# Optimization experiments

Hardware: AMD Instinct MI355X
Metric: run time of the kernel (lower is better)

## Reference

```python
import jax, jax.numpy as jnp
import numpy as np

N = 50000
H = 300


def l2_normalize(x, eps=1e-12):
    n = jnp.sqrt(jnp.sum(x * x, axis=1, keepdims=True))
    return x / jnp.maximum(n, eps)


def gat_layer(x, ei_j, ei_i, a_i, a_j, n_nodes):
    # per-node scalar scores, gathered per edge
    s_i = x @ a_i  # [N]
    s_j = x @ a_j  # [N]
    e = jax.nn.leaky_relu(s_i[ei_i] + s_j[ei_j], 0.01)  # [E]
    # scatter softmax over incoming edges of node i
    m = jax.ops.segment_max(e, ei_i, num_segments=n_nodes)
    ex = jnp.exp(e - m[ei_i])
    denom = jax.ops.segment_sum(ex, ei_i, num_segments=n_nodes)
    alpha = ex / (denom[ei_i] + 1e-16)
    out = jax.ops.segment_sum(alpha[:, None] * x[ei_j], ei_i, num_segments=n_nodes)
    return jax.nn.relu(out)


def gcn_layer(x, ei_j, ei_i, W, n_nodes):
    deg = jax.ops.segment_sum(jnp.ones_like(ei_i, dtype=x.dtype), ei_i, num_segments=n_nodes)
    dinv = jnp.where(deg > 0, deg ** -0.5, 0.0)
    norm = dinv[ei_j] * dinv[ei_i]  # [E]
    h = x @ W.T
    out = jax.ops.segment_sum(norm[:, None] * h[ei_j], ei_i, num_segments=n_nodes)
    return jax.nn.relu(out)


def highway(x1, x2, W, b):
    gate = jax.nn.sigmoid(x1 @ W.T + b)
    return gate * x2 + (1.0 - gate) * x1


def setup_inputs() -> dict:
    key = jax.random.key(0)
    ks = jax.random.split(key, 16)
    s = 1.0 / np.sqrt(H)
    inp = {
        "x_e": jax.random.normal(ks[0], (N, H), dtype=jnp.float32),
        "edge_index": jax.random.randint(ks[1], (2, 400000), 0, N, dtype=jnp.int32),
        "rel": jax.random.randint(ks[2], (400000,), 0, 1000, dtype=jnp.int32),
        "edge_index_all": jax.random.randint(ks[3], (2, 800000), 0, N, dtype=jnp.int32),
        "rel_all": jax.random.randint(ks[4], (800000,), 0, 1000, dtype=jnp.int32),
        "gcn1_W": jax.random.uniform(ks[5], (H, H), jnp.float32, -s, s),
        "hw1_W": jax.random.uniform(ks[6], (H, H), jnp.float32, -s, s),
        "hw1_b": jax.random.uniform(ks[7], (H,), jnp.float32, -s, s),
        "gat1_ai": jax.random.uniform(ks[8], (H,), jnp.float32, -s, s),
        "gat1_aj": jax.random.uniform(ks[9], (H,), jnp.float32, -s, s),
        "ghw1_W": jax.random.uniform(ks[10], (H, H), jnp.float32, -s, s),
        "ghw1_b": jax.random.uniform(ks[11], (H,), jnp.float32, -s, s),
        "gat2_ai": jax.random.uniform(ks[12], (H,), jnp.float32, -s, s),
        "gat2_aj": jax.random.uniform(ks[13], (H,), jnp.float32, -s, s),
        "ghw2_W": jax.random.uniform(ks[14], (H, H), jnp.float32, -s, s),
        "ghw2_b": jax.random.uniform(ks[15], (H,), jnp.float32, -s, s),
    }
    k2 = jax.random.split(jax.random.key(1), 2)
    inp["gat_ai"] = jax.random.uniform(k2[0], (H,), jnp.float32, -s, s)
    inp["gat_aj"] = jax.random.uniform(k2[1], (H,), jnp.float32, -s, s)
    return inp


def reference(x_e, edge_index, rel, edge_index_all, rel_all,
              gcn1_W, hw1_W, hw1_b, gat1_ai, gat1_aj, ghw1_W, ghw1_b,
              gat2_ai, gat2_aj, ghw2_W, ghw2_b, gat_ai, gat_aj):
    # dropout(p=0.05) treated as identity (eval mode)
    ei_j, ei_i = edge_index_all[0], edge_index_all[1]
    n = x_e.shape[0]

    x0 = l2_normalize(x_e)
    x2 = highway(x0, gcn_layer(x0, ei_j, ei_i, gcn1_W, n), hw1_W, hw1_b)
    x3 = highway(x2, gat_layer(x2, ei_j, ei_i, gat1_ai, gat1_aj, n), ghw1_W, ghw1_b)
    xe = highway(x2, gat_layer(x3, ei_j, ei_i, gat2_ai, gat2_aj, n), ghw2_W, ghw2_b)
    ye = gat_layer(xe, ei_j, ei_i, gat_ai, gat_aj, n)
    return jnp.concatenate([xe, ye], axis=1)
```

## Files before the change

### kernel.cpp

```cpp
#include <hip/hip_runtime.h>
#include <hip/hip_bf16.h>
#include <math.h>

#define H 300
#define WAVE 64
#define STRB 320
#define SCB 1024

typedef short bf16x8 __attribute__((ext_vector_type(8)));
typedef unsigned short u16;
typedef u16 u16x8 __attribute__((ext_vector_type(8)));
typedef u16 u16x4 __attribute__((ext_vector_type(4)));
typedef float f32x4 __attribute__((ext_vector_type(4)));

__device__ inline unsigned short f2b(float f) {
    union { float f; unsigned int u; } x; x.f = f;
    unsigned int r = x.u + 0x7FFF + ((x.u >> 16) & 1);
    return (unsigned short)(r >> 16);
}
__device__ inline float b2f(u16 h) {
    union { float f; unsigned int u; } x; x.u = ((unsigned int)h) << 16;
    return x.f;
}

__global__ void k_l2norm(const float* __restrict__ x, u16* __restrict__ outb, int n) {
    int wave = blockIdx.x * (blockDim.x / WAVE) + (threadIdx.x >> 6);
    int lane = threadIdx.x & 63;
    if (wave >= n) return;
    const float* row = x + (long)wave * H;
    float s = 0.f;
    for (int j = lane; j < H; j += WAVE) { float v = row[j]; s += v * v; }
    for (int o = 32; o > 0; o >>= 1) s += __shfl_xor(s, o);
    float sc = 1.0f / fmaxf(sqrtf(s), 1e-12f);
    u16* brow = outb + (long)wave * STRB;
    for (int j = lane; j < H; j += WAVE) brow[j] = f2b(row[j] * sc);
    for (int j = H + lane; j < STRB; j += WAVE) brow[j] = 0;
}

__global__ void k_zero_int(int* p, int n) {
    int i = blockIdx.x * blockDim.x + threadIdx.x;
    int stride = gridDim.x * blockDim.x;
    for (; i < n; i += stride) p[i] = 0;
}

__global__ void k_count_deg(const int* __restrict__ ei_i, int* __restrict__ deg, int E) {
    int i = blockIdx.x * blockDim.x + threadIdx.x;
    int stride = gridDim.x * blockDim.x;
    for (; i < E; i += stride) atomicAdd(&deg[ei_i[i]], 1);
}

__global__ void k_scan_local(const int* __restrict__ deg, int* __restrict__ offs,
                             int* __restrict__ btot, float* __restrict__ dinv, int n) {
    __shared__ int sh[SCB];
    int base = blockIdx.x * SCB;
    int tid = threadIdx.x;
    int v = (base + tid < n) ? deg[base + tid] : 0;
    if (base + tid < n) dinv[base + tid] = (v > 0) ? 1.0f / sqrtf((float)v) : 0.0f;
    sh[tid] = v;
    __syncthreads();
    for (int off = 1; off < SCB; off <<= 1) {
        int add = (tid >= off) ? sh[tid - off] : 0;
        __syncthreads();
        sh[tid] += add;
        __syncthreads();
    }
    if (base + tid < n) offs[base + tid] = sh[tid] - v;
    if (tid == SCB - 1) btot[blockIdx.x] = sh[tid];
}

__global__ void k_scan_tots(const int* __restrict__ btot, int* __restrict__ bpre,
                            int nb, int* __restrict__ total_out) {
    int l = threadIdx.x;
    int v = (l < nb) ? btot[l] : 0;
    int own = v;
    for (int o = 1; o < 64; o <<= 1) {
        int u = __shfl_up(v, o);
        if (l >= o) v += u;
    }
    if (l < nb) bpre[l] = v - own;
    if (l == 63) total_out[0] = v;
}

__global__ void k_scan_apply(int* __restrict__ offs, const int* __restrict__ bpre,
                             int* __restrict__ cursor, int n) {
    int i = blockIdx.x * blockDim.x + threadIdx.x;
    int stride = gridDim.x * blockDim.x;
    for (; i < n; i += stride) {
        int o = offs[i] + bpre[i / SCB];
        offs[i] = o;
        cursor[i] = o;
    }
}

__global__ void k_fill_csr(const int* __restrict__ ei_j, const int* __restrict__ ei_i,
                           int* __restrict__ cursor, int* __restrict__ csr_src, int E) {
    int i = blockIdx.x * blockDim.x + threadIdx.x;
    int stride = gridDim.x * blockDim.x;
    for (; i < E; i += stride) {
        int dst = ei_i[i];
        int pos = atomicAdd(&cursor[dst], 1);
        csr_src[pos] = ei_j[i];
    }
}

__global__ void k_conv_w4(const float* __restrict__ W0f, const float* __restrict__ W1f,
                          const float* __restrict__ W2f, const float* __restrict__ W3f,
                          u16* __restrict__ Wb0, u16* __restrict__ Wb1,
                          u16* __restrict__ Wb2, u16* __restrict__ Wb3) {
    int which = blockIdx.x & 3;
    const float* W = (which == 0) ? W0f : (which == 1) ? W1f : (which == 2) ? W2f : W3f;
    u16* Wb = (which == 0) ? Wb0 : (which == 1) ? Wb1 : (which == 2) ? Wb2 : Wb3;
    int idx = (blockIdx.x >> 2) * blockDim.x + threadIdx.x;
    int stride = (gridDim.x >> 2) * blockDim.x;
    for (; idx < STRB * STRB; idx += stride) {
        int r = idx / STRB, c = idx - r * STRB;
        Wb[idx] = (r < H && c < H) ? f2b(W[r * H + c]) : 0;
    }
}

#define BM 128
#define BN 64
#define BK 32
#define LDP 40
#define STP 70
#define NXCD 8

__global__ __launch_bounds__(256) void k_gemm_fused(
        const u16* __restrict__ Xb,
        const u16* __restrict__ Wb,
        u16* __restrict__ outb,
        const float* __restrict__ hwbias,
        const u16* __restrict__ xnewb, const float* __restrict__ xnewf,
        const u16* __restrict__ xold,
        float* __restrict__ outf, long ostride,
        u16* __restrict__ mirror,
        int n_rows) {
    __shared__ __align__(16) char smem[BM * STP * 2];
    short* As = (short*)smem;
    short* Bs = (short*)(smem + BM * LDP * 2);
    u16*   St = (u16*)smem;
    const int tid = threadIdx.x;

    const int nwg = gridDim.x;
    const int q = nwg / NXCD, r = nwg % NXCD;
    const int xcd = blockIdx.x % NXCD, idx = blockIdx.x / NXCD;
    const int wgid = (xcd < r ? xcd * (q + 1) : r * (q + 1) + (xcd - r) * q) + idx;
    const int bm = (wgid / 5) * BM;
    const int bn = (wgid % 5) * BN;

    const int lane = tid & 63;
    const int wid = tid >> 6;
    const int wr = wid >> 1;
    const int wc = wid & 1;
    const int lrow = lane & 15;
    const int kgrp = lane >> 4;

    f32x4 acc[4][2];
    #pragma unroll
    for (int m = 0; m < 4; m++)
        #pragma unroll
        for (int n = 0; n < 2; n++) acc[m][n] = (f32x4){0.f, 0.f, 0.f, 0.f};

    for (int k0 = 0; k0 < STRB; k0 += BK) {
        #pragma unroll
        for (int i = 0; i < 2; ++i) {
            int qq = tid + i * 256;
            int rr = qq >> 2, c = (qq & 3) << 3;
            int gr = bm + rr;
            u16x8 v = {0, 0, 0, 0, 0, 0, 0, 0};
            if (gr < n_rows) v = *(const u16x8*)&Xb[(long)gr * STRB + k0 + c];
            *(u16x8*)&As[rr * LDP + c] = v;
        }
        {
            int rr = tid >> 2, c = (tid & 3) << 3;
            u16x8 v = *(const u16x8*)&Wb[(long)(bn + rr) * STRB + k0 + c];
            *(u16x8*)&Bs[rr * LDP + c] = v;
        }
        __syncthreads();

        bf16x8 af[4], bfr[2];
        #pragma unroll
        for (int m = 0; m < 4; m++) {
            int row = wr * 64 + m * 16 + lrow;
            af[m] = *(const bf16x8*)&As[row * LDP + kgrp * 8];
        }
        #pragma unroll
        for (int n = 0; n < 2; n++) {
            int col = wc * 32 + n * 16 + lrow;
            bfr[n] = *(const bf16x8*)&Bs[col * LDP + kgrp * 8];
        }
        #pragma unroll
        for (int m = 0; m < 4; m++)
            #pragma unroll
            for (int n = 0; n < 2; n++)
                acc[m][n] = __builtin_amdgcn_mfma_f32_16x16x32_bf16(af[m], bfr[n], acc[m][n], 0, 0, 0);
        __syncthreads();
    }

    #pragma unroll
    for (int m = 0; m < 4; m++)
        #pragma unroll
        for (int n = 0; n < 2; n++) {
            int lc = wc * 32 + n * 16 + lrow;
            #pragma unroll
            for (int rr = 0; rr < 4; rr++) {
                int row = wr * 64 + m * 16 + kgrp * 4 + rr;
                St[row * STP + lc] = f2b(acc[m][n][rr]);
            }
        }
    __syncthreads();

    #pragma unroll
    for (int p = 0; p < 4; p++) {
        int row = p * 32 + (tid >> 3);
        int gr = bm + row;
        if (gr >= n_rows) continue;
        int lc0 = (tid & 7) * 8;
        int gc0 = bn + lc0;
        u16x8 pv = *(const u16x8*)&St[row * STP + lc0];
        if (outb) {
            u16x8 o;
            #pragma unroll
            for (int j = 0; j < 8; j++) o[j] = (gc0 + j < H) ? pv[j] : (u16)0;
            *(u16x8*)&outb[(long)gr * STRB + gc0] = o;
        } else {
            u16x8 xov = *(const u16x8*)&xold[(long)gr * STRB + gc0];
            float xn[8];
            if (xnewb) {
                u16x8 xnv = *(const u16x8*)&xnewb[(long)gr * STRB + gc0];
                #pragma unroll
                for (int j = 0; j < 8; j++) xn[j] = b2f(xnv[j]);
            } else {
                f32x4 a = *(const f32x4*)&xnewf[(long)gr * H + gc0];
                f32x4 b = *(const f32x4*)&xnewf[(long)gr * H + gc0 + 4];
                xn[0] = a[0]; xn[1] = a[1]; xn[2] = a[2]; xn[3] = a[3];
                xn[4] = b[0]; xn[5] = b[1]; xn[6] = b[2]; xn[7] = b[3];
            }
            float val[8];
            #pragma unroll
            for (int j = 0; j < 8; j++) {
                int gcj = gc0 + j;
                if (gcj < H) {
                    float pre = b2f(pv[j]) + hwbias[gcj];
                    float g = 1.0f / (1.0f + __expf(-pre));
                    val[j] = g * xn[j] + (1.0f - g) * b2f(xov[j]);
                } else val[j] = 0.f;
            }
            if (outf) {
                if (gc0 < H)
                    *(f32x4*)&outf[(long)gr * ostride + gc0] = (f32x4){val[0], val[1], val[2], val[3]};
                if (gc0 + 4 < H)
                    *(f32x4*)&outf[(long)gr * ostride + gc0 + 4] = (f32x4){val[4], val[5], val[6], val[7]};
            }
            if (mirror) {
                u16x8 mv;
                #pragma unroll
                for (int j = 0; j < 8; j++) mv[j] = f2b(val[j]);
                *(u16x8*)&mirror[(long)gr * STRB + gc0] = mv;
            }
        }
    }
}

__global__ __launch_bounds__(256) void k_gcn_gather_w(const u16* __restrict__ xb,
                                                      const float* __restrict__ dinv,
                                                      const int* __restrict__ offs,
                                                      const int* __restrict__ csr,
                                                      u16* __restrict__ outb, int n) {
    int node = blockIdx.x * 4 + (threadIdx.x >> 6);
    int lane = threadIdx.x & 63;
    if (node >= n) return;
    int start = offs[node], end = offs[node + 1];
    float acc[8];
    #pragma unroll
    for (int j = 0; j < 8; j++) acc[j] = 0.f;
    float di = dinv[node];
    for (int tb = start; tb < end; tb += 64) {
        int p = tb + lane;
        int src = 0; float w = 0.f;
        if (p < end) {
            src = csr[p];
            w = di * dinv[src];
        }
        int cnt = min(64, end - tb);
        for (int qq = 0; qq < cnt; qq++) {
            float wq = __shfl(w, qq);
            int sq = __shfl(src, qq);
            if (lane < 40) {
                u16x8 v = *(const u16x8*)&xb[(long)sq * STRB + lane * 8];
                #pragma unroll
                for (int j = 0; j < 8; j++) acc[j] += wq * b2f(v[j]);
            }
        }
    }
    if (lane < 40) {
        u16x8 o;
        #pragma unroll
        for (int j = 0; j < 8; j++) o[j] = f2b(fmaxf(acc[j], 0.f));
        *(u16x8*)&outb[(long)node * STRB + lane * 8] = o;
    }
}

__global__ void k_dual_dot_b(const u16* __restrict__ xb,
                             const float* __restrict__ ai, const float* __restrict__ aj,
                             float* __restrict__ s_i, float* __restrict__ s_j, int n) {
    int wave = blockIdx.x * (blockDim.x / WAVE) + (threadIdx.x >> 6);
    int lane = threadIdx.x & 63;
    if (wave >= n) return;
    const u16* row = xb + (long)wave * STRB;
    float d0 = 0.f, d1 = 0.f;
    {
        u16x4 v = *(const u16x4*)&row[lane * 4];
        float4 a4 = *(const float4*)&ai[lane * 4];
        float4 j4 = *(const float4*)&aj[lane * 4];
        float x0 = b2f(v[0]), x1 = b2f(v[1]), x2 = b2f(v[2]), x3 = b2f(v[3]);
        d0 = x0 * a4.x + x1 * a4.y + x2 * a4.z + x3 * a4.w;
        d1 = x0 * j4.x + x1 * j4.y + x2 * j4.z + x3 * j4.w;
    }
    if (lane < 11) {
        u16x4 v = *(const u16x4*)&row[256 + lane * 4];
        float4 a4 = *(const float4*)&ai[256 + lane * 4];
        float4 j4 = *(const float4*)&aj[256 + lane * 4];
        float x0 = b2f(v[0]), x1 = b2f(v[1]), x2 = b2f(v[2]), x3 = b2f(v[3]);
        d0 += x0 * a4.x + x1 * a4.y + x2 * a4.z + x3 * a4.w;
        d1 += x0 * j4.x + x1 * j4.y + x2 * j4.z + x3 * j4.w;
    }
    for (int o = 32; o > 0; o >>= 1) { d0 += __shfl_down(d0, o); d1 += __shfl_down(d1, o); }
    if (lane == 0) { s_i[wave] = d0; s_j[wave] = d1; }
}

__global__ __launch_bounds__(256) void k_gat_gather_w(const u16* __restrict__ xb,
                                                      const float* __restrict__ s_i_arr,
                                                      const float* __restrict__ s_j_arr,
                                                      const int* __restrict__ offs,
                                                      const int* __restrict__ csr,
                                                      u16* __restrict__ outb16,
                                                      float* __restrict__ outf, long out_stride,
                                                      int out_off, int n) {
    int node = blockIdx.x * 4 + (threadIdx.x >> 6);
    int lane = threadIdx.x & 63;
    if (node >= n) return;
    int start = offs[node], end = offs[node + 1];
    int deg = end - start;
    float acc[8];
    #pragma unroll
    for (int j = 0; j < 8; j++) acc[j] = 0.f;

    if (deg > 0) {
        float si = s_i_arr[node];
        float m_t = -1e30f, s_t = 0.f;
        for (int p = start + lane; p < end; p += 64) {
            float sc = si + s_j_arr[csr[p]];
            sc = (sc >= 0.f) ? sc : 0.01f * sc;
            if (sc > m_t) { s_t = s_t * __expf(m_t - sc) + 1.0f; m_t = sc; }
            else s_t += __expf(sc - m_t);
        }
        for (int o = 32; o > 0; o >>= 1) {
            float m2 = __shfl_xor(m_t, o), s2 = __shfl_xor(s_t, o);
            float mm = fmaxf(m_t, m2);
            s_t = s_t * __expf(m_t - mm) + s2 * __expf(m2 - mm);
            m_t = mm;
        }
        float m = m_t;
        float inv = 1.0f / (s_t + 1e-16f);
        for (int tb = start; tb < end; tb += 64) {
            int p = tb + lane;
            int src = 0; float w = 0.f;
            if (p < end) {
                src = csr[p];
                float sc = si + s_j_arr[src];
                sc = (sc >= 0.f) ? sc : 0.01f * sc;
                w = __expf(sc - m) * inv;
            }
            int cnt = min(64, end - tb);
            for (int qq = 0; qq < cnt; qq++) {
                float wq = __shfl(w, qq);
                int sq = __shfl(src, qq);
                if (lane < 40) {
                    u16x8 v = *(const u16x8*)&xb[(long)sq * STRB + lane * 8];
                    #pragma unroll
                    for (int j = 0; j < 8; j++) acc[j] += wq * b2f(v[j]);
                }
            }
        }
    }
    if (outb16) {
        if (lane < 40) {
            u16x8 o;
            #pragma unroll
            for (int j = 0; j < 8; j++) o[j] = f2b(fmaxf(acc[j], 0.f));
            *(u16x8*)&outb16[(long)node * STRB + lane * 8] = o;
        }
    } else {
        if (lane < 38) {
            #pragma unroll
            for (int j = 0; j < 8; j++) {
                int c = lane * 8 + j;
                if (c < H) outf[(long)node * out_stride + out_off + c] = fmaxf(acc[j], 0.f);
            }
        }
    }
}

extern "C" void kernel_launch(void* const* d_in, const int* in_sizes, int n_in,
                              void* d_out, int out_size, void* d_ws, size_t ws_size,
                              hipStream_t stream) {
    const float* x_e     = (const float*)d_in[0];
    const int*   ei_all  = (const int*)d_in[3];
    const float* gcn1_W  = (const float*)d_in[5];
    const float* hw1_W   = (const float*)d_in[6];
    const float* hw1_b   = (const float*)d_in[7];
    const float* gat1_ai = (const float*)d_in[8];
    const float* gat1_aj = (const float*)d_in[9];
    const float* ghw1_W  = (const float*)d_in[10];
    const float* ghw1_b  = (const float*)d_in[11];
    const float* gat2_ai = (const float*)d_in[12];
    const float* gat2_aj = (const float*)d_in[13];
    const float* ghw2_W  = (const float*)d_in[14];
    const float* ghw2_b  = (const float*)d_in[15];
    const float* gat_ai  = (const float*)d_in[16];
    const float* gat_aj  = (const float*)d_in[17];

    const int N = in_sizes[0] / H;
    const int E = in_sizes[3] / 2;
    const int* ei_j = ei_all;
    const int* ei_i = ei_all + E;

    float* out = (float*)d_out;

    size_t NSB = (size_t)N * STRB;
    u16*   W0   = (u16*)d_ws;
    u16*   W1   = W0 + NSB;
    u16*   W2   = W1 + NSB;
    u16*   W3   = W2 + NSB;
    float* G2F  = (float*)d_ws;
    float* sbi  = (float*)(W3 + NSB);
    float* sbj  = sbi + N;
    float* dinv = sbj + N;
    int*   deg  = (int*)(dinv + N);
    int*   offs = deg + N;
    int*   cursor = offs + (N + 1);
    int*   csr  = cursor + N;
    int*   btot = csr + E;
    int*   bpre = btot + 64;
    u16*   wb0  = (u16*)(bpre + 64);
    u16*   wb1  = wb0 + STRB * STRB;
    u16*   wb2  = wb1 + STRB * STRB;
    u16*   wb3  = wb2 + STRB * STRB;

    dim3 blk256(256);
    int rowsPerBlock = 256 / WAVE;
    dim3 gridRows((N + rowsPerBlock - 1) / rowsPerBlock);
    dim3 gridNodeW((N + 3) / 4);
    dim3 gridE(2048);
    dim3 gridW(400);
    dim3 gridGemm(((N + BM - 1) / BM) * 5);
    int nScanB = (N + SCB - 1) / SCB;

    hipLaunchKernelGGL(k_l2norm, gridRows, blk256, 0, stream, x_e, W0, N);

    hipLaunchKernelGGL(k_zero_int, dim3(256), blk256, 0, stream, deg, N);
    hipLaunchKernelGGL(k_count_deg, gridE, blk256, 0, stream, ei_i, deg, E);
    hipLaunchKernelGGL(k_scan_local, dim3(nScanB), dim3(SCB), 0, stream, deg, offs, btot, dinv, N);
    hipLaunchKernelGGL(k_scan_tots, dim3(1), dim3(64), 0, stream, btot, bpre, nScanB, offs + N);
    hipLaunchKernelGGL(k_scan_apply, dim3(256), blk256, 0, stream, offs, bpre, cursor, N);
    hipLaunchKernelGGL(k_fill_csr, gridE, blk256, 0, stream, ei_j, ei_i, cursor, csr, E);
    hipLaunchKernelGGL(k_conv_w4, gridW, blk256, 0, stream,
                       gcn1_W, hw1_W, ghw1_W, ghw2_W, wb0, wb1, wb2, wb3);

    hipLaunchKernelGGL(k_gemm_fused, gridGemm, blk256, 0, stream,
                       W0, wb0, W1,
                       (const float*)nullptr, (const u16*)nullptr, (const float*)nullptr,
                       (const u16*)nullptr, (float*)nullptr, (long)0, (u16*)nullptr, N);

    hipLaunchKernelGGL(k_gcn_gather_w, gridNodeW, blk256, 0, stream, W1, dinv, offs, csr, W2, N);

    hipLaunchKernelGGL(k_gemm_fused, gridGemm, blk256, 0, stream,
                       W0, wb1, (u16*)nullptr,
                       hw1_b, W2, (const float*)nullptr, W0,
                       (float*)nullptr, (long)0, W3, N);

    hipLaunchKernelGGL(k_dual_dot_b, gridRows, blk256, 0, stream, W3, gat1_ai, gat1_aj, sbi, sbj, N);

    hipLaunchKernelGGL(k_gat_gather_w, gridNodeW, blk256, 0, stream, W3, sbi, sbj, offs, csr,
                       W1, (float*)nullptr, (long)0, 0, N);

    hipLaunchKernelGGL(k_gemm_fused, gridGemm, blk256, 0, stream,
                       W3, wb2, (u16*)nullptr,
                       ghw1_b, W1, (const float*)nullptr, W3,
                       (float*)nullptr, (long)0, W2, N);

    hipLaunchKernelGGL(k_dual_dot_b, gridRows, blk256, 0, stream, W2, gat2_ai, gat2_aj, sbi, sbj, N);

    hipLaunchKernelGGL(k_gat_gather_w, gridNodeW, blk256, 0, stream, W2, sbi, sbj, offs, csr,
                       (u16*)nullptr, G2F, (long)H, 0, N);

    hipLaunchKernelGGL(k_gemm_fused, gridGemm, blk256, 0, stream,
                       W3, wb3, (u16*)nullptr,
                       ghw2_b, (const u16*)nullptr, G2F, W3,
                       out, (long)(2 * H), W2, N);

    hipLaunchKernelGGL(k_dual_dot_b, gridRows, blk256, 0, stream, W2, gat_ai, gat_aj, sbi, sbj, N);

    hipLaunchKernelGGL(k_gat_gather_w, gridNodeW, blk256, 0, stream, W2, sbi, sbj, offs, csr,
                       (u16*)nullptr, out, (long)(2 * H), H, N);
}
```

Measured before the change: 693.0 us.

## Fuse GAT score dot products into GEMM epilogue and unroll gather loops

Computes the per-node attention scores s_i/s_j inside the highway GEMM epilogue via partial dot products, shuffle reductions and atomicAdd into zeroed buffers. This removes the separate dual-dot kernels that reread the bf16 feature matrix. The GCN and GAT neighbour gather loops are also unrolled by four so that several row loads are in flight at once. The cost is extra memsets, atomic traffic and higher register pressure in the gather kernels.

```diff
diff --git a/kernel.cpp b/kernel.cpp
--- a/kernel.cpp
+++ b/kernel.cpp
@@ -10,7 +10,6 @@
 typedef short bf16x8 __attribute__((ext_vector_type(8)));
 typedef unsigned short u16;
 typedef u16 u16x8 __attribute__((ext_vector_type(8)));
-typedef u16 u16x4 __attribute__((ext_vector_type(4)));
 typedef float f32x4 __attribute__((ext_vector_type(4)));
 
 __device__ inline unsigned short f2b(float f) {
@@ -134,6 +133,8 @@
         const u16* __restrict__ xold,
         float* __restrict__ outf, long ostride,
         u16* __restrict__ mirror,
+        const float* __restrict__ dai, const float* __restrict__ daj,
+        float* __restrict__ sbi, float* __restrict__ sbj,
         int n_rows) {
     __shared__ __align__(16) char smem[BM * STP * 2];
     short* As = (short*)smem;
@@ -258,6 +259,26 @@
                 for (int j = 0; j < 8; j++) mv[j] = f2b(val[j]);
                 *(u16x8*)&mirror[(long)gr * STRB + gc0] = mv;
             }
+            if (dai) {
+                float p0 = 0.f, p1 = 0.f;
+                #pragma unroll
+                for (int j = 0; j < 8; j++) {
+                    int gcj = gc0 + j;
+                    if (gcj < H) {
+                        p0 += val[j] * dai[gcj];
+                        p1 += val[j] * daj[gcj];
+                    }
+                }
+                #pragma unroll
+                for (int o = 4; o > 0; o >>= 1) {
+                    p0 += __shfl_down(p0, o);
+                    p1 += __shfl_down(p1, o);
+                }
+                if ((tid & 7) == 0) {
+                    atomicAdd(&sbi[gr], p0);
+                    atomicAdd(&sbj[gr], p1);
+                }
+            }
         }
     }
 }
@@ -275,6 +296,7 @@
     #pragma unroll
     for (int j = 0; j < 8; j++) acc[j] = 0.f;
     float di = dinv[node];
+    const u16* rowp = xb + lane * 8;
     for (int tb = start; tb < end; tb += 64) {
         int p = tb + lane;
         int src = 0; float w = 0.f;
@@ -283,11 +305,32 @@
             w = di * dinv[src];
         }
         int cnt = min(64, end - tb);
-        for (int qq = 0; qq < cnt; qq++) {
+        int qq = 0;
+        for (; qq + 4 <= cnt; qq += 4) {
+            float w0 = __shfl(w, qq), w1 = __shfl(w, qq + 1);
+            float w2 = __shfl(w, qq + 2), w3 = __shfl(w, qq + 3);
+            int s0 = __shfl(src, qq), s1 = __shfl(src, qq + 1);
+            int s2 = __shfl(src, qq + 2), s3 = __shfl(src, qq + 3);
+            if (lane < 40) {
+                u16x8 v0 = *(const u16x8*)&rowp[(long)s0 * STRB];
+                u16x8 v1 = *(const u16x8*)&rowp[(long)s1 * STRB];
+                u16x8 v2 = *(const u16x8*)&rowp[(long)s2 * STRB];
+                u16x8 v3 = *(const u16x8*)&rowp[(long)s3 * STRB];
+                #pragma unroll
+                for (int j = 0; j < 8; j++) acc[j] += w0 * b2f(v0[j]);
+                #pragma unroll
+                for (int j = 0; j < 8; j++) acc[j] += w1 * b2f(v1[j]);
+                #pragma unroll
+                for (int j = 0; j < 8; j++) acc[j] += w2 * b2f(v2[j]);
+                #pragma unroll
+                for (int j = 0; j < 8; j++) acc[j] += w3 * b2f(v3[j]);
+            }
+        }
+        for (; qq < cnt; qq++) {
             float wq = __shfl(w, qq);
             int sq = __shfl(src, qq);
             if (lane < 40) {
-                u16x8 v = *(const u16x8*)&xb[(long)sq * STRB + lane * 8];
+                u16x8 v = *(const u16x8*)&rowp[(long)sq * STRB];
                 #pragma unroll
                 for (int j = 0; j < 8; j++) acc[j] += wq * b2f(v[j]);
             }
@@ -299,34 +342,6 @@
         for (int j = 0; j < 8; j++) o[j] = f2b(fmaxf(acc[j], 0.f));
         *(u16x8*)&outb[(long)node * STRB + lane * 8] = o;
     }
-}
-
-__global__ void k_dual_dot_b(const u16* __restrict__ xb,
-                             const float* __restrict__ ai, const float* __restrict__ aj,
-                             float* __restrict__ s_i, float* __restrict__ s_j, int n) {
-    int wave = blockIdx.x * (blockDim.x / WAVE) + (threadIdx.x >> 6);
-    int lane = threadIdx.x & 63;
-    if (wave >= n) return;
-    const u16* row = xb + (long)wave * STRB;
-    float d0 = 0.f, d1 = 0.f;
-    {
-        u16x4 v = *(const u16x4*)&row[lane * 4];
-        float4 a4 = *(const float4*)&ai[lane * 4];
-        float4 j4 = *(const float4*)&aj[lane * 4];
-        float x0 = b2f(v[0]), x1 = b2f(v[1]), x2 = b2f(v[2]), x3 = b2f(v[3]);
-        d0 = x0 * a4.x + x1 * a4.y + x2 * a4.z + x3 * a4.w;
-        d1 = x0 * j4.x + x1 * j4.y + x2 * j4.z + x3 * j4.w;
-    }
-    if (lane < 11) {
-        u16x4 v = *(const u16x4*)&row[256 + lane * 4];
-        float4 a4 = *(const float4*)&ai[256 + lane * 4];
-        float4 j4 = *(const float4*)&aj[256 + lane * 4];
-        float x0 = b2f(v[0]), x1 = b2f(v[1]), x2 = b2f(v[2]), x3 = b2f(v[3]);
-        d0 += x0 * a4.x + x1 * a4.y + x2 * a4.z + x3 * a4.w;
-        d1 += x0 * j4.x + x1 * j4.y + x2 * j4.z + x3 * j4.w;
-    }
-    for (int o = 32; o > 0; o >>= 1) { d0 += __shfl_down(d0, o); d1 += __shfl_down(d1, o); }
-    if (lane == 0) { s_i[wave] = d0; s_j[wave] = d1; }
 }
 
 __global__ __launch_bounds__(256) void k_gat_gather_w(const u16* __restrict__ xb,
@@ -363,6 +378,7 @@
         }
         float m = m_t;
         float inv = 1.0f / (s_t + 1e-16f);
+        const u16* rowp = xb + lane * 8;
         for (int tb = start; tb < end; tb += 64) {
             int p = tb + lane;
             int src = 0; float w = 0.f;
@@ -373,11 +389,32 @@
                 w = __expf(sc - m) * inv;
             }
             int cnt = min(64, end - tb);
-            for (int qq = 0; qq < cnt; qq++) {
+            int qq = 0;
+            for (; qq + 4 <= cnt; qq += 4) {
+                float w0 = __shfl(w, qq), w1 = __shfl(w, qq + 1);
+                float w2 = __shfl(w, qq + 2), w3 = __shfl(w, qq + 3);
+                int s0 = __shfl(src, qq), s1 = __shfl(src, qq + 1);
+                int s2 = __shfl(src, qq + 2), s3 = __shfl(src, qq + 3);
+                if (lane < 40) {
+                    u16x8 v0 = *(const u16x8*)&rowp[(long)s0 * STRB];
+                    u16x8 v1 = *(const u16x8*)&rowp[(long)s1 * STRB];
+                    u16x8 v2 = *(const u16x8*)&rowp[(long)s2 * STRB];
+                    u16x8 v3 = *(const u16x8*)&rowp[(long)s3 * STRB];
+                    #pragma unroll
+                    for (int j = 0; j < 8; j++) acc[j] += w0 * b2f(v0[j]);
+                    #pragma unroll
+                    for (int j = 0; j < 8; j++) acc[j] += w1 * b2f(v1[j]);
+                    #pragma unroll
+                    for (int j = 0; j < 8; j++) acc[j] += w2 * b2f(v2[j]);
+                    #pragma unroll
+                    for (int j = 0; j < 8; j++) acc[j] += w3 * b2f(v3[j]);
+                }
+            }
+            for (; qq < cnt; qq++) {
                 float wq = __shfl(w, qq);
                 int sq = __shfl(src, qq);
                 if (lane < 40) {
-                    u16x8 v = *(const u16x8*)&xb[(long)sq * STRB + lane * 8];
+                    u16x8 v = *(const u16x8*)&rowp[(long)sq * STRB];
                     #pragma unroll
                     for (int j = 0; j < 8; j++) acc[j] += wq * b2f(v[j]);
                 }
@@ -471,36 +508,38 @@
     hipLaunchKernelGGL(k_gemm_fused, gridGemm, blk256, 0, stream,
                        W0, wb0, W1,
                        (const float*)nullptr, (const u16*)nullptr, (const float*)nullptr,
-                       (const u16*)nullptr, (float*)nullptr, (long)0, (u16*)nullptr, N);
+                       (const u16*)nullptr, (float*)nullptr, (long)0, (u16*)nullptr,
+                       (const float*)nullptr, (const float*)nullptr,
+                       (float*)nullptr, (float*)nullptr, N);
 
     hipLaunchKernelGGL(k_gcn_gather_w, gridNodeW, blk256, 0, stream, W1, dinv, offs, csr, W2, N);
 
+    hipMemsetAsync(sbi, 0, 2 * (size_t)N * sizeof(float), stream);
     hipLaunchKernelGGL(k_gemm_fused, gridGemm, blk256, 0, stream,
                        W0, wb1, (u16*)nullptr,
                        hw1_b, W2, (const float*)nullptr, W0,
-                       (float*)nullptr, (long)0, W3, N);
-
-    hipLaunchKernelGGL(k_dual_dot_b, gridRows, blk256, 0, stream, W3, gat1_ai, gat1_aj, sbi, sbj, N);
+                       (float*)nullptr, (long)0, W3,
+                       gat1_ai, gat1_aj, sbi, sbj, N);
 
     hipLaunchKernelGGL(k_gat_gather_w, gridNodeW, blk256, 0, stream, W3, sbi, sbj, offs, csr,
                        W1, (float*)nullptr, (long)0, 0, N);
 
+    hipMemsetAsync(sbi, 0, 2 * (size_t)N * sizeof(float), stream);
     hipLaunchKernelGGL(k_gemm_fused, gridGemm, blk256, 0, stream,
                        W3, wb2, (u16*)nullptr,
                        ghw1_b, W1, (const float*)nullptr, W3,
-                       (float*)nullptr, (long)0, W2, N);
-
-    hipLaunchKernelGGL(k_dual_dot_b, gridRows, blk256, 0, stream, W2, gat2_ai, gat2_aj, sbi, sbj, N);
+                       (float*)nullptr, (long)0, W2,
+                       gat2_ai, gat2_aj, sbi, sbj, N);
 
     hipLaunchKernelGGL(k_gat_gather_w, gridNodeW, blk256, 0, stream, W2, sbi, sbj, offs, csr,
                        (u16*)nullptr, G2F, (long)H, 0, N);
 
+    hipMemsetAsync(sbi, 0, 2 * (size_t)N * sizeof(float), stream);
     hipLaunchKernelGGL(k_gemm_fused, gridGemm, blk256, 0, stream,
                        W3, wb3, (u16*)nullptr,
                        ghw2_b, (const u16*)nullptr, G2F, W3,
-                       out, (long)(2 * H), W2, N);
-
-    hipLaunchKernelGGL(k_dual_dot_b, gridRows, blk256, 0, stream, W2, gat_ai, gat_aj, sbi, sbj, N);
+                       out, (long)(2 * H), W2,
+                       gat_ai, gat_aj, sbi, sbj, N);
 
     hipLaunchKernelGGL(k_gat_gather_w, gridNodeW, blk256, 0, stream, W2, sbi, sbj, offs, csr,
                        (u16*)nullptr, out, (long)(2 * H), H, N);
```

Result: no change. 706.5 us (+1.9%).

## Split each wave into four edge slots in GCN/GAT gather kernels

Applied to the files above, without the earlier changes.

The GCN and GAT neighbour-gather kernels now split each 64-lane wave into four 16-lane slots. Each slot processes a different edge, and each lane covers 20 feature columns. Previously only 40 lanes did work and edges were processed one at a time. The partial sums are then reduced across slots with two xor shuffles, and slot 0 writes the row, using vectorized f32x4 stores for the float output. This aims to use all lanes and keep more row fetches in flight. The costs are narrower 8-byte loads, a larger accumulator footprint, and an extra cross-lane reduction per node.

```diff
diff --git a/kernel.cpp b/kernel.cpp
--- a/kernel.cpp
+++ b/kernel.cpp
@@ -271,10 +271,15 @@
     int lane = threadIdx.x & 63;
     if (node >= n) return;
     int start = offs[node], end = offs[node + 1];
-    float acc[8];
-    #pragma unroll
-    for (int j = 0; j < 8; j++) acc[j] = 0.f;
+    int slot = lane >> 4;
+    int ce = (lane & 15) * 20;
+    float acc[5][4];
+    #pragma unroll
+    for (int k = 0; k < 5; k++)
+        #pragma unroll
+        for (int j = 0; j < 4; j++) acc[k][j] = 0.f;
     float di = dinv[node];
+    const u16* basep = xb + ce;
     for (int tb = start; tb < end; tb += 64) {
         int p = tb + lane;
         int src = 0; float w = 0.f;
@@ -283,21 +288,48 @@
             w = di * dinv[src];
         }
         int cnt = min(64, end - tb);
-        for (int qq = 0; qq < cnt; qq++) {
-            float wq = __shfl(w, qq);
-            int sq = __shfl(src, qq);
-            if (lane < 40) {
-                u16x8 v = *(const u16x8*)&xb[(long)sq * STRB + lane * 8];
-                #pragma unroll
-                for (int j = 0; j < 8; j++) acc[j] += wq * b2f(v[j]);
-            }
-        }
-    }
-    if (lane < 40) {
-        u16x8 o;
-        #pragma unroll
-        for (int j = 0; j < 8; j++) o[j] = f2b(fmaxf(acc[j], 0.f));
-        *(u16x8*)&outb[(long)node * STRB + lane * 8] = o;
+        for (int qb = 0; qb < cnt; qb += 4) {
+            int myq = qb + slot;
+            float wq = __shfl(w, myq);
+            int sq = __shfl(src, myq);
+            if (myq < cnt) {
+                const u16* row = basep + (long)sq * STRB;
+                u16x4 v0 = *(const u16x4*)(row);
+                u16x4 v1 = *(const u16x4*)(row + 4);
+                u16x4 v2 = *(const u16x4*)(row + 8);
+                u16x4 v3 = *(const u16x4*)(row + 12);
+                u16x4 v4 = *(const u16x4*)(row + 16);
+                #pragma unroll
+                for (int j = 0; j < 4; j++) acc[0][j] += wq * b2f(v0[j]);
+                #pragma unroll
+                for (int j = 0; j < 4; j++) acc[1][j] += wq * b2f(v1[j]);
+                #pragma unroll
+                for (int j = 0; j < 4; j++) acc[2][j] += wq * b2f(v2[j]);
+                #pragma unroll
+                for (int j = 0; j < 4; j++) acc[3][j] += wq * b2f(v3[j]);
+                #pragma unroll
+                for (int j = 0; j < 4; j++) acc[4][j] += wq * b2f(v4[j]);
+            }
+        }
+    }
+    #pragma unroll
+    for (int k = 0; k < 5; k++)
+        #pragma unroll
+        for (int j = 0; j < 4; j++) {
+            float v = acc[k][j];
+            v += __shfl_xor(v, 16);
+            v += __shfl_xor(v, 32);
+            acc[k][j] = v;
+        }
+    if (slot == 0) {
+        u16* orow = outb + (long)node * STRB + ce;
+        #pragma unroll
+        for (int k = 0; k < 5; k++) {
+            u16x4 o;
+            #pragma unroll
+            for (int j = 0; j < 4; j++) o[j] = f2b(fmaxf(acc[k][j], 0.f));
+            *(u16x4*)(orow + k * 4) = o;
+        }
     }
 }
 
@@ -342,9 +374,13 @@
     if (node >= n) return;
     int start = offs[node], end = offs[node + 1];
     int deg = end - start;
-    float acc[8];
-    #pragma unroll
-    for (int j = 0; j < 8; j++) acc[j] = 0.f;
+    int slot = lane >> 4;
+    int ce = (lane & 15) * 20;
+    float acc[5][4];
+    #pragma unroll
+    for (int k = 0; k < 5; k++)
+        #pragma unroll
+        for (int j = 0; j < 4; j++) acc[k][j] = 0.f;
 
     if (deg > 0) {
         float si = s_i_arr[node];
@@ -363,6 +399,7 @@
         }
         float m = m_t;
         float inv = 1.0f / (s_t + 1e-16f);
+        const u16* basep = xb + ce;
         for (int tb = start; tb < end; tb += 64) {
             int p = tb + lane;
             int src = 0; float w = 0.f;
@@ -373,30 +410,60 @@
                 w = __expf(sc - m) * inv;
             }
             int cnt = min(64, end - tb);
-            for (int qq = 0; qq < cnt; qq++) {
-                float wq = __shfl(w, qq);
-                int sq = __shfl(src, qq);
-                if (lane < 40) {
-                    u16x8 v = *(const u16x8*)&xb[(long)sq * STRB + lane * 8];
+            for (int qb = 0; qb < cnt; qb += 4) {
+                int myq = qb + slot;
+                float wq = __shfl(w, myq);
+                int sq = __shfl(src, myq);
+                if (myq < cnt) {
+                    const u16* row = basep + (long)sq * STRB;
+                    u16x4 v0 = *(const u16x4*)(row);
+                    u16x4 v1 = *(const u16x4*)(row + 4);
+                    u16x4 v2 = *(const u16x4*)(row + 8);
+                    u16x4 v3 = *(const u16x4*)(row + 12);
+                    u16x4 v4 = *(const u16x4*)(row + 16);
                     #pragma unroll
-                    for (int j = 0; j < 8; j++) acc[j] += wq * b2f(v[j]);
+                    for (int j = 0; j < 4; j++) acc[0][j] += wq * b2f(v0[j]);
+                    #pragma unroll
+                    for (int j = 0; j < 4; j++) acc[1][j] += wq * b2f(v1[j]);
+                    #pragma unroll
+                    for (int j = 0; j < 4; j++) acc[2][j] += wq * b2f(v2[j]);
+                    #pragma unroll
+                    for (int j = 0; j < 4; j++) acc[3][j] += wq * b2f(v3[j]);
+                    #pragma unroll
+                    for (int j = 0; j < 4; j++) acc[4][j] += wq * b2f(v4[j]);
                 }
             }
         }
     }
-    if (outb16) {
-        if (lane < 40) {
-            u16x8 o;
-            #pragma unroll
-            for (int j = 0; j < 8; j++) o[j] = f2b(fmaxf(acc[j], 0.f));
-            *(u16x8*)&outb16[(long)node * STRB + lane * 8] = o;
-        }
-    } else {
-        if (lane < 38) {
-            #pragma unroll
-            for (int j = 0; j < 8; j++) {
-                int c = lane * 8 + j;
-                if (c < H) outf[(long)node * out_stride + out_off + c] = fmaxf(acc[j], 0.f);
+    #pragma unroll
+    for (int k = 0; k < 5; k++)
+        #pragma unroll
+        for (int j = 0; j < 4; j++) {
+            float v = acc[k][j];
+            v += __shfl_xor(v, 16);
+            v += __shfl_xor(v, 32);
+            acc[k][j] = v;
+        }
+    if (slot == 0) {
+        if (outb16) {
+            u16* orow = outb16 + (long)node * STRB + ce;
+            #pragma unroll
+            for (int k = 0; k < 5; k++) {
+                u16x4 o;
+                #pragma unroll
+                for (int j = 0; j < 4; j++) o[j] = f2b(fmaxf(acc[k][j], 0.f));
+                *(u16x4*)(orow + k * 4) = o;
+            }
+        } else {
+            float* orow = outf + (long)node * out_stride + out_off;
+            #pragma unroll
+            for (int k = 0; k < 5; k++) {
+                int c0 = ce + k * 4;
+                if (c0 < H) {
+                    f32x4 o = (f32x4){fmaxf(acc[k][0], 0.f), fmaxf(acc[k][1], 0.f),
+                                      fmaxf(acc[k][2], 0.f), fmaxf(acc[k][3], 0.f)};
+                    *(f32x4*)(orow + c0) = o;
+                }
             }
         }
     }
```

New measurement: 661.8 us. 4.5% less time.
